# Performance work log

Hardware: AMD Instinct MI355X
Metric: run time of the kernel (lower is better)

The kernel has to match this reference:

```python
import jax, jax.numpy as jnp
import numpy as np

H = 1024
L = 2

def setup_inputs() -> dict:
    key = jax.random.key(0)
    k1, k2, k3, k4, k5 = jax.random.split(key, 5)
    B, S = 32, 2048
    scale = 1.0 / np.sqrt(H)
    return {
        "query": jax.random.normal(k1, (B, 1, H * L), dtype=jnp.float32),
        "keys": jax.random.normal(k2, (B, S, H), dtype=jnp.float32),
        "Wa_w": jax.random.normal(k3, (H * L, H), dtype=jnp.float32) * scale,
        "Wa_b": jnp.zeros((H,), dtype=jnp.float32),
        "Ua_w": jax.random.normal(k4, (H, H), dtype=jnp.float32) * scale,
        "Ua_b": jnp.zeros((H,), dtype=jnp.float32),
        "Va_w": jax.random.normal(k5, (H, 1), dtype=jnp.float32) * scale,
        "Va_b": jnp.zeros((1,), dtype=jnp.float32),
    }

def reference(query, keys, Wa_w, Wa_b, Ua_w, Ua_b, Va_w, Va_b):
    # query: [B,1,H*L], keys: [B,S,H]
    q = jnp.einsum('bqd,dh->bqh', query, Wa_w) + Wa_b   # [B,1,H]
    k = jnp.einsum('bsd,dh->bsh', keys, Ua_w) + Ua_b    # [B,S,H]
    e = jnp.tanh(q + k)                                  # [B,S,H]
    scores = jnp.einsum('bsh,ho->bso', e, Va_w) + Va_b   # [B,S,1]
    scores = scores[:, :, 0][:, None, :]                 # [B,1,S]
    weights = jax.nn.softmax(scores, axis=-1)            # [B,1,S]
    context = jnp.einsum('bqs,bsh->bqh', weights, keys)  # [B,1,H]
    return (context, weights)
```

## Files before the change

### kernel.cpp

```cpp
#include <hip/hip_runtime.h>
#include <hip/hip_bf16.h>


typedef __attribute__((ext_vector_type(8))) short short8;
typedef __attribute__((ext_vector_type(4))) float floatx4;

__device__ __forceinline__ unsigned short f2bf(float f) {
    union { float f; unsigned int u; } c; c.f = f;
    unsigned int u = c.u + 0x7fffu + ((c.u >> 16) & 1u);
    return (unsigned short)(u >> 16);
}

__global__ __launch_bounds__(256) void qproj_k(
    const float* __restrict__ query, const float* __restrict__ Wa,
    const float* __restrict__ Wab, const float* __restrict__ Uab,
    float* __restrict__ qws)
{
    __shared__ float qs[2048];
    __shared__ float red[4][64];
    const int tid = threadIdx.x;
    const int b = blockIdx.x, hc = blockIdx.y;
    #pragma unroll
    for (int i = 0; i < 8; i++) qs[tid + 256*i] = query[b*2048 + tid + 256*i];
    __syncthreads();
    const int h_l = tid & 63, dg = tid >> 6;
    const int h = hc*64 + h_l;
    float acc = 0.f;
    const float* wp = Wa + (size_t)(dg*512)*1024 + h;
    const float* qp = qs + dg*512;
    #pragma unroll 4
    for (int d = 0; d < 512; d++) acc += qp[d] * wp[(size_t)d*1024];
    red[dg][h_l] = acc;
    __syncthreads();
    if (tid < 64) {
        float r = red[0][tid] + red[1][tid] + red[2][tid] + red[3][tid];
        int hh = hc*64 + tid;
        qws[b*1024 + hh] = r + Wab[hh] + Uab[hh];
    }
}

__global__ __launch_bounds__(256) void uat_k(const float* __restrict__ Ua,
                                             unsigned short* __restrict__ uat)
{
    __shared__ unsigned short t[64][65];
    const int x = threadIdx.x & 63, yy = threadIdx.x >> 6;
    const int d0 = blockIdx.x*64, h0 = blockIdx.y*64;
    #pragma unroll
    for (int i = 0; i < 16; i++) {
        int y = yy*16 + i;
        t[y][x] = f2bf(Ua[(size_t)(d0+y)*1024 + h0 + x]);
    }
    __syncthreads();
    #pragma unroll
    for (int i = 0; i < 16; i++) {
        int y = yy*16 + i;
        uat[(size_t)(h0+y)*1024 + d0 + x] = t[x][y];
    }
}

__global__ __launch_bounds__(256) void score_gemm(
    const float* __restrict__ keys,
    const unsigned short* __restrict__ uat,
    const float* __restrict__ qws,
    const float* __restrict__ Va,
    float* __restrict__ partial)
{
    __shared__ unsigned short aS[128][40];
    __shared__ unsigned short bS[128][40];
    const int tid = threadIdx.x;
    const int b = blockIdx.z;
    const int s0 = blockIdx.x * 128;
    const int h0 = blockIdx.y * 128;
    const int lane = tid & 63, wave = tid >> 6;
    const int quad = lane >> 4, l15 = lane & 15;
    const int wm = (wave & 1) * 64, wn = (wave >> 1) * 64;

    floatx4 acc[4][4];
    #pragma unroll
    for (int i = 0; i < 4; i++)
        #pragma unroll
        for (int j = 0; j < 4; j++) acc[i][j] = (floatx4)0.0f;

    const float4* keys4 = reinterpret_cast<const float4*>(keys) + (size_t)(b*2048 + s0)*256;
    const uint4*  uat4  = reinterpret_cast<const uint4*>(uat) + (size_t)h0*128;

    for (int k0 = 0; k0 < 1024; k0 += 32) {
        #pragma unroll
        for (int i = 0; i < 4; i++) {
            int f = tid + 256*i;
            int row = f >> 3, c4 = f & 7;
            float4 v = keys4[(size_t)row*256 + (k0 >> 2) + c4];
            ushort4 o;
            o.x = f2bf(v.x); o.y = f2bf(v.y); o.z = f2bf(v.z); o.w = f2bf(v.w);
            *reinterpret_cast<ushort4*>(&aS[row][c4*4]) = o;
        }
        #pragma unroll
        for (int i = 0; i < 2; i++) {
            int f = tid + 256*i;
            int row = f >> 2, c8 = f & 3;
            uint4 v = uat4[(size_t)row*128 + (k0 >> 3) + c8];
            *reinterpret_cast<uint4*>(&bS[row][c8*8]) = v;
        }
        __syncthreads();
        short8 af[4], bf8[4];
        #pragma unroll
        for (int i = 0; i < 4; i++)
            af[i] = *reinterpret_cast<const short8*>(&aS[wm + 16*i + l15][quad*8]);
        #pragma unroll
        for (int j = 0; j < 4; j++)
            bf8[j] = *reinterpret_cast<const short8*>(&bS[wn + 16*j + l15][quad*8]);
        #pragma unroll
        for (int i = 0; i < 4; i++)
            #pragma unroll
            for (int j = 0; j < 4; j++)
                acc[i][j] = __builtin_amdgcn_mfma_f32_16x16x32_bf16(af[i], bf8[j], acc[i][j], 0, 0, 0);
        __syncthreads();
    }

    float qv[4], vav[4];
    #pragma unroll
    for (int j = 0; j < 4; j++) {
        int n = h0 + wn + 16*j + l15;
        qv[j]  = qws[b*1024 + n];
        vav[j] = Va[n];
    }
    const int slot = blockIdx.y * 2 + (wave >> 1);
    #pragma unroll
    for (int i = 0; i < 4; i++) {
        #pragma unroll
        for (int r = 0; r < 4; r++) {
            float p = 0.f;
            #pragma unroll
            for (int j = 0; j < 4; j++) {
                float x = qv[j] + acc[i][j][r];
                float e = __expf(2.f * x);
                float t = 1.f - 2.f * __builtin_amdgcn_rcpf(e + 1.f);
                p += vav[j] * t;
            }
            #pragma unroll
            for (int off = 1; off < 16; off <<= 1) p += __shfl_xor(p, off, 64);
            if (l15 == 0) {
                int m = wm + 16*i + quad*4 + r;
                partial[((size_t)b*16 + slot)*2048 + s0 + m] = p;
            }
        }
    }
}

__global__ __launch_bounds__(256) void softmax_k(const float* __restrict__ partial,
                                                 float* __restrict__ out_w)
{
    const int tid = threadIdx.x;
    const int b = blockIdx.x;
    __shared__ float wred[4], wred2[4];
    float sc[8];
    float mx = -3.0e38f;
    #pragma unroll
    for (int i = 0; i < 8; i++) {
        int s = tid + 256*i;
        float v = 0.f;
        #pragma unroll
        for (int ht = 0; ht < 16; ht++) v += partial[((size_t)b*16 + ht)*2048 + s];
        sc[i] = v; mx = fmaxf(mx, v);
    }
    #pragma unroll
    for (int off = 32; off >= 1; off >>= 1) mx = fmaxf(mx, __shfl_xor(mx, off, 64));
    if ((tid & 63) == 0) wred[tid >> 6] = mx;
    __syncthreads();
    mx = fmaxf(fmaxf(wred[0], wred[1]), fmaxf(wred[2], wred[3]));
    float e[8]; float lsum = 0.f;
    #pragma unroll
    for (int i = 0; i < 8; i++) { e[i] = __expf(sc[i] - mx); lsum += e[i]; }
    #pragma unroll
    for (int off = 32; off >= 1; off >>= 1) lsum += __shfl_xor(lsum, off, 64);
    if ((tid & 63) == 0) wred2[tid >> 6] = lsum;
    __syncthreads();
    float inv = 1.0f / (wred2[0] + wred2[1] + wred2[2] + wred2[3]);
    #pragma unroll
    for (int i = 0; i < 8; i++) out_w[b*2048 + tid + 256*i] = e[i] * inv;
}

__global__ __launch_bounds__(256) void ctx_k(const float* __restrict__ keys,
                                             const float* __restrict__ w,
                                             float* __restrict__ ctxp)
{
    const int tid = threadIdx.x;
    const int b = blockIdx.x, sc = blockIdx.y;
    const float4* k4 = reinterpret_cast<const float4*>(keys) + (size_t)(b*2048 + sc*256)*256;
    const float* wp = w + b*2048 + sc*256;
    float4 a; a.x = a.y = a.z = a.w = 0.f;
    #pragma unroll 4
    for (int s = 0; s < 256; s++) {
        float wv = wp[s];
        float4 kv = k4[(size_t)s*256 + tid];
        a.x += wv*kv.x; a.y += wv*kv.y; a.z += wv*kv.z; a.w += wv*kv.w;
    }
    reinterpret_cast<float4*>(ctxp)[((size_t)b*8 + sc)*256 + tid] = a;
}

__global__ __launch_bounds__(256) void ctxsum_k(const float* __restrict__ ctxp,
                                                float* __restrict__ out)
{
    const int idx = blockIdx.x*256 + threadIdx.x;
    const int b = idx >> 10, h = idx & 1023;
    float v = 0.f;
    #pragma unroll
    for (int sc = 0; sc < 8; sc++) v += ctxp[((size_t)b*8 + sc)*1024 + h];
    out[idx] = v;
}

extern "C" void kernel_launch(void* const* d_in, const int* in_sizes, int n_in,
                              void* d_out, int out_size, void* d_ws, size_t ws_size,
                              hipStream_t stream)
{
    const float* query = (const float*)d_in[0];
    const float* keys  = (const float*)d_in[1];
    const float* Wa_w  = (const float*)d_in[2];
    const float* Wa_b  = (const float*)d_in[3];
    const float* Ua_w  = (const float*)d_in[4];
    const float* Ua_b  = (const float*)d_in[5];
    const float* Va_w  = (const float*)d_in[6];

    char* ws = (char*)d_ws;
    float*          qws     = (float*)(ws);
    unsigned short* uat     = (unsigned short*)(ws + 131072);
    float*          partial = (float*)(ws + 131072 + 2097152);
    float*          ctxp    = (float*)(ws + 131072 + 2097152 + 4194304);

    float* out_ctx = (float*)d_out;
    float* out_w   = out_ctx + 32*1024;

    qproj_k  <<<dim3(32, 16),    256, 0, stream>>>(query, Wa_w, Wa_b, Ua_b, qws);
    uat_k    <<<dim3(16, 16),    256, 0, stream>>>(Ua_w, uat);
    score_gemm<<<dim3(16, 8, 32), 256, 0, stream>>>(keys, uat, qws, Va_w, partial);
    softmax_k<<<dim3(32),        256, 0, stream>>>(partial, out_w);
    ctx_k    <<<dim3(32, 8),     256, 0, stream>>>(keys, out_w, ctxp);
    ctxsum_k <<<dim3(128),       256, 0, stream>>>(ctxp, out_ctx);
}
```

Before: 689.2 us.

## Use direct global-to-LDS loads, swizzled LDS, packed bf16 convert, vectorized qproj, finer ctx split

The score GEMM now loads the bf16 Ua^T tile straight into LDS with global_load_lds and uses an XOR-swizzled unpadded LDS layout to avoid bank conflicts. Keys are converted with a packed bf16 conversion builtin when available. The query projection is rewritten to use float4 weight loads with a 16-way d split, and the context reduction uses 16 chunks instead of 8 for more parallelism. Together these target global load and LDS overheads in the dominant GEMM and occupancy in the small kernels. The cost is more complex indexing, plus a dependence on the direct-to-LDS load builtin and the swizzle being correct.

```diff
diff --git a/kernel.cpp b/kernel.cpp
--- a/kernel.cpp
+++ b/kernel.cpp
@@ -4,6 +4,9 @@
 
 typedef __attribute__((ext_vector_type(8))) short short8;
 typedef __attribute__((ext_vector_type(4))) float floatx4;
+
+typedef const __attribute__((address_space(1))) unsigned int gu32;
+typedef __attribute__((address_space(3))) unsigned int lu32;
 
 __device__ __forceinline__ unsigned short f2bf(float f) {
     union { float f; unsigned int u; } c; c.f = f;
@@ -11,31 +14,58 @@
     return (unsigned short)(u >> 16);
 }
 
+__device__ __forceinline__ unsigned int f2bf2(float lo, float hi) {
+#if __has_builtin(__builtin_amdgcn_cvt_pk_bf16_f32)
+    auto r = __builtin_amdgcn_cvt_pk_bf16_f32(lo, hi);
+    unsigned int u; __builtin_memcpy(&u, &r, 4);
+    return u;
+#else
+    return (unsigned int)f2bf(lo) | ((unsigned int)f2bf(hi) << 16);
+#endif
+}
+
+__device__ __forceinline__ void gld16(const unsigned short* g, unsigned short* l) {
+    __builtin_amdgcn_global_load_lds(
+        (gu32*)(uintptr_t)g,
+        (lu32*)(unsigned int)(uintptr_t)l,
+        16, 0, 0);
+}
+
 __global__ __launch_bounds__(256) void qproj_k(
     const float* __restrict__ query, const float* __restrict__ Wa,
     const float* __restrict__ Wab, const float* __restrict__ Uab,
     float* __restrict__ qws)
 {
     __shared__ float qs[2048];
-    __shared__ float red[4][64];
+    __shared__ float red[16*64];
     const int tid = threadIdx.x;
     const int b = blockIdx.x, hc = blockIdx.y;
     #pragma unroll
     for (int i = 0; i < 8; i++) qs[tid + 256*i] = query[b*2048 + tid + 256*i];
     __syncthreads();
-    const int h_l = tid & 63, dg = tid >> 6;
-    const int h = hc*64 + h_l;
-    float acc = 0.f;
-    const float* wp = Wa + (size_t)(dg*512)*1024 + h;
-    const float* qp = qs + dg*512;
+    const int hq = tid & 15;
+    const int dg = tid >> 4;
+    const float4* wp = reinterpret_cast<const float4*>(Wa + (size_t)(dg*128)*1024 + hc*64 + hq*4);
+    const float* qp = qs + dg*128;
+    float4 a0; a0.x = a0.y = a0.z = a0.w = 0.f;
+    float4 a1; a1.x = a1.y = a1.z = a1.w = 0.f;
     #pragma unroll 4
-    for (int d = 0; d < 512; d++) acc += qp[d] * wp[(size_t)d*1024];
-    red[dg][h_l] = acc;
+    for (int d = 0; d < 128; d += 2) {
+        float q0 = qp[d], q1 = qp[d+1];
+        float4 w0 = wp[(size_t)d*256];
+        float4 w1 = wp[(size_t)(d+1)*256];
+        a0.x += q0*w0.x; a0.y += q0*w0.y; a0.z += q0*w0.z; a0.w += q0*w0.w;
+        a1.x += q1*w1.x; a1.y += q1*w1.y; a1.z += q1*w1.z; a1.w += q1*w1.w;
+    }
+    a0.x += a1.x; a0.y += a1.y; a0.z += a1.z; a0.w += a1.w;
+    *reinterpret_cast<float4*>(red + dg*64 + hq*4) = a0;
     __syncthreads();
     if (tid < 64) {
-        float r = red[0][tid] + red[1][tid] + red[2][tid] + red[3][tid];
+        float v = 0.f;
+        #pragma unroll
+        for (int g = 0; g < 16; g++) v += red[g*64 + tid];
         int hh = hc*64 + tid;
-        qws[b*1024 + hh] = r + Wab[hh] + Uab[hh];
+        qws[b*1024 + hh] = v + Wab[hh] + Uab[hh];
     }
 }
 
@@ -58,15 +88,15 @@
     }
 }
 
-__global__ __launch_bounds__(256) void score_gemm(
+__global__ __launch_bounds__(256) void score_gemm_fast(
     const float* __restrict__ keys,
     const unsigned short* __restrict__ uat,
     const float* __restrict__ qws,
     const float* __restrict__ Va,
     float* __restrict__ partial)
 {
-    __shared__ unsigned short aS[128][40];
-    __shared__ unsigned short bS[128][40];
+    __shared__ unsigned short aS[128*32];
+    __shared__ unsigned short bS[128*32];
     const int tid = threadIdx.x;
     const int b = blockIdx.z;
     const int s0 = blockIdx.x * 128;
@@ -75,40 +105,50 @@
     const int quad = lane >> 4, l15 = lane & 15;
     const int wm = (wave & 1) * 64, wn = (wave >> 1) * 64;
 
+    const int srow = lane >> 2;
+    const int schunk = (lane & 3) ^ ((srow >> 1) & 3);
+
     floatx4 acc[4][4];
     #pragma unroll
     for (int i = 0; i < 4; i++)
         #pragma unroll
         for (int j = 0; j < 4; j++) acc[i][j] = (floatx4)0.0f;
 
-    const float4* keys4 = reinterpret_cast<const float4*>(keys) + (size_t)(b*2048 + s0)*256;
-    const uint4*  uat4  = reinterpret_cast<const uint4*>(uat) + (size_t)h0*128;
+    const float* kA = keys + (size_t)(b*2048 + s0)*1024;
+    const unsigned short* ubase = uat + (size_t)h0*1024;
+    const int c0 = wave*2, c1 = wave*2 + 1;
+    const size_t boff0 = (size_t)(c0*16 + srow)*1024 + schunk*8;
+    const size_t boff1 = (size_t)(c1*16 + srow)*1024 + schunk*8;
+
+    const int arow0 = tid >> 2, ac = tid & 3;
 
     for (int k0 = 0; k0 < 1024; k0 += 32) {
-        #pragma unroll
-        for (int i = 0; i < 4; i++) {
-            int f = tid + 256*i;
-            int row = f >> 3, c4 = f & 7;
-            float4 v = keys4[(size_t)row*256 + (k0 >> 2) + c4];
-            ushort4 o;
-            o.x = f2bf(v.x); o.y = f2bf(v.y); o.z = f2bf(v.z); o.w = f2bf(v.w);
-            *reinterpret_cast<ushort4*>(&aS[row][c4*4]) = o;
-        }
+        gld16(ubase + boff0 + k0, bS + c0*512);
+        gld16(ubase + boff1 + k0, bS + c1*512);
         #pragma unroll
         for (int i = 0; i < 2; i++) {
-            int f = tid + 256*i;
-            int row = f >> 2, c8 = f & 3;
-            uint4 v = uat4[(size_t)row*128 + (k0 >> 3) + c8];
-            *reinterpret_cast<uint4*>(&bS[row][c8*8]) = v;
+            int row = arow0 + 64*i;
+            int sl  = ac ^ ((row >> 1) & 3);
+            const float* gp = kA + (size_t)row*1024 + k0 + ac*8;
+            float4 v0 = *reinterpret_cast<const float4*>(gp);
+            float4 v1 = *reinterpret_cast<const float4*>(gp + 4);
+            uint4 w;
+            w.x = f2bf2(v0.x, v0.y); w.y = f2bf2(v0.z, v0.w);
+            w.z = f2bf2(v1.x, v1.y); w.w = f2bf2(v1.z, v1.w);
+            *reinterpret_cast<uint4*>(aS + row*32 + sl*8) = w;
         }
         __syncthreads();
         short8 af[4], bf8[4];
         #pragma unroll
-        for (int i = 0; i < 4; i++)
-            af[i] = *reinterpret_cast<const short8*>(&aS[wm + 16*i + l15][quad*8]);
-        #pragma unroll
-        for (int j = 0; j < 4; j++)
-            bf8[j] = *reinterpret_cast<const short8*>(&bS[wn + 16*j + l15][quad*8]);
+        for (int i = 0; i < 4; i++) {
+            int row = wm + 16*i + l15;
+            af[i] = *reinterpret_cast<const short8*>(aS + row*32 + ((quad ^ ((row>>1)&3)) * 8));
+        }
+        #pragma unroll
+        for (int j = 0; j < 4; j++) {
+            int row = wn + 16*j + l15;
+            bf8[j] = *reinterpret_cast<const short8*>(bS + row*32 + ((quad ^ ((row>>1)&3)) * 8));
+        }
         #pragma unroll
         for (int i = 0; i < 4; i++)
             #pragma unroll
@@ -182,30 +222,29 @@
 
 __global__ __launch_bounds__(256) void ctx_k(const float* __restrict__ keys,
                                              const float* __restrict__ w,
-                                             float* __restrict__ ctxp)
+                                             float* __restrict__ ctxp, int sper)
 {
     const int tid = threadIdx.x;
     const int b = blockIdx.x, sc = blockIdx.y;
-    const float4* k4 = reinterpret_cast<const float4*>(keys) + (size_t)(b*2048 + sc*256)*256;
-    const float* wp = w + b*2048 + sc*256;
+    const float4* k4 = reinterpret_cast<const float4*>(keys) + (size_t)(b*2048 + sc*sper)*256;
+    const float* wp = w + b*2048 + sc*sper;
     float4 a; a.x = a.y = a.z = a.w = 0.f;
     #pragma unroll 4
-    for (int s = 0; s < 256; s++) {
+    for (int s = 0; s < sper; s++) {
         float wv = wp[s];
         float4 kv = k4[(size_t)s*256 + tid];
         a.x += wv*kv.x; a.y += wv*kv.y; a.z += wv*kv.z; a.w += wv*kv.w;
     }
-    reinterpret_cast<float4*>(ctxp)[((size_t)b*8 + sc)*256 + tid] = a;
+    reinterpret_cast<float4*>(ctxp)[((size_t)b*gridDim.y + sc)*256 + tid] = a;
 }
 
 __global__ __launch_bounds__(256) void ctxsum_k(const float* __restrict__ ctxp,
-                                                float* __restrict__ out)
+                                                float* __restrict__ out, int nc)
 {
     const int idx = blockIdx.x*256 + threadIdx.x;
     const int b = idx >> 10, h = idx & 1023;
     float v = 0.f;
-    #pragma unroll
-    for (int sc = 0; sc < 8; sc++) v += ctxp[((size_t)b*8 + sc)*1024 + h];
+    for (int s = 0; s < nc; s++) v += ctxp[((size_t)b*nc + s)*1024 + h];
     out[idx] = v;
 }
 
@@ -223,17 +262,17 @@
 
     char* ws = (char*)d_ws;
     float*          qws     = (float*)(ws);
-    unsigned short* uat     = (unsigned short*)(ws + 131072);
-    float*          partial = (float*)(ws + 131072 + 2097152);
-    float*          ctxp    = (float*)(ws + 131072 + 2097152 + 4194304);
+    unsigned short* uat     = (unsigned short*)(ws + (131072));
+    float*          partial = (float*)(ws + (131072 + 2097152));
+    float*          ctxp    = (float*)(ws + (131072 + 2097152 + 4194304));
 
     float* out_ctx = (float*)d_out;
     float* out_w   = out_ctx + 32*1024;
 
-    qproj_k  <<<dim3(32, 16),    256, 0, stream>>>(query, Wa_w, Wa_b, Ua_b, qws);
-    uat_k    <<<dim3(16, 16),    256, 0, stream>>>(Ua_w, uat);
-    score_gemm<<<dim3(16, 8, 32), 256, 0, stream>>>(keys, uat, qws, Va_w, partial);
-    softmax_k<<<dim3(32),        256, 0, stream>>>(partial, out_w);
-    ctx_k    <<<dim3(32, 8),     256, 0, stream>>>(keys, out_w, ctxp);
-    ctxsum_k <<<dim3(128),       256, 0, stream>>>(ctxp, out_ctx);
-}
+    qproj_k        <<<dim3(32, 16),    256, 0, stream>>>(query, Wa_w, Wa_b, Ua_b, qws);
+    uat_k          <<<dim3(16, 16),    256, 0, stream>>>(Ua_w, uat);
+    score_gemm_fast<<<dim3(16, 8, 32), 256, 0, stream>>>(keys, uat, qws, Va_w, partial);
+    softmax_k      <<<dim3(32),        256, 0, stream>>>(partial, out_w);
+    ctx_k          <<<dim3(32, 16),    256, 0, stream>>>(keys, out_w, ctxp, 128);
+    ctxsum_k       <<<dim3(128),       256, 0, stream>>>(ctxp, out_ctx, 16);
+}
```

After: 659.4 us. 4.3% less time.
